# Performance work log

Measured on AMD Instinct MI355X. Metric: run time of the kernel, lower is better.

The kernel has to match this reference:

```python
import jax, jax.numpy as jnp
import numpy as np

DIM = 1024
HIDDEN = 4096
NUM_EXPERTS = 8
TOP_K = 2
T = 8192


def setup_inputs() -> dict:
    key = jax.random.key(0)
    ks = jax.random.split(key, 5)
    scale = 0.02
    x = jax.random.normal(ks[0], (T, DIM), dtype=jnp.float32)
    gate_w = jax.random.normal(ks[1], (NUM_EXPERTS, DIM), dtype=jnp.float32) * scale  # Linear weight [out,in]
    w1 = jax.random.normal(ks[2], (NUM_EXPERTS, HIDDEN, DIM), dtype=jnp.float32) * scale
    w2 = jax.random.normal(ks[3], (NUM_EXPERTS, DIM, HIDDEN), dtype=jnp.float32) * scale
    w3 = jax.random.normal(ks[4], (NUM_EXPERTS, HIDDEN, DIM), dtype=jnp.float32) * scale
    return {"x": x, "gate_w": gate_w, "w1": w1, "w2": w2, "w3": w3}


def reference(x, gate_w, w1, w2, w3):
    # Router: softmax over all experts, take top-2, renormalize.
    logits = jnp.einsum('td,ed->te', x, gate_w)            # [T, E]
    probs = jax.nn.softmax(logits, axis=-1)
    topw, topi = jax.lax.top_k(probs, TOP_K)               # [T, 2]
    topw = topw / jnp.sum(topw, axis=-1, keepdims=True)
    out = jnp.zeros_like(x)
    num_experts = w1.shape[0]
    for e in range(num_experts):
        # combine weight for expert e per token (0 if not routed here)
        w_e = jnp.sum(jnp.where(topi == e, topw, 0.0), axis=-1)   # [T]
        h = jax.nn.silu(x @ w1[e].T) * (x @ w3[e].T)              # [T, HIDDEN]
        out = out + w_e[:, None] * (h @ w2[e].T)                  # [T, DIM]
    return out
```

## Files before the change

### kernel.cpp

```cpp
#include <hip/hip_runtime.h>
#include <hip/hip_bf16.h>
#include <cstdint>
#include <cstddef>

#define TK 8192
#define DIM 1024
#define HID 4096
#define NE 8

#define BK 64
#define NIT1 (DIM / BK)
#define NIT2 (HID / BK)
#define HSZ 4096

typedef __attribute__((ext_vector_type(8))) __bf16 bfrag;
typedef __attribute__((ext_vector_type(4))) float ffrag;

static __device__ __forceinline__ ushort f2bf(float f) {
    union { float f; uint32_t u; } v; v.f = f;
    uint32_t r = (v.u + 0x7fffu + ((v.u >> 16) & 1u)) >> 16;
    return (ushort)r;
}

static __device__ __forceinline__ uint4 pack8(float4 a, float4 b) {
    union { ushort u[8]; uint4 q; } pk;
    pk.u[0] = f2bf(a.x); pk.u[1] = f2bf(a.y); pk.u[2] = f2bf(a.z); pk.u[3] = f2bf(a.w);
    pk.u[4] = f2bf(b.x); pk.u[5] = f2bf(b.y); pk.u[6] = f2bf(b.z); pk.u[7] = f2bf(b.w);
    return pk.q;
}

static __device__ __forceinline__ void gld16(const ushort* g, ushort* l) {
    __builtin_amdgcn_global_load_lds(
        (const __attribute__((address_space(1))) unsigned int*)g,
        (__attribute__((address_space(3))) unsigned int*)l, 16, 0, 0);
}

#define LDSIDX(r, kc) ((((r) >> 3) << 8) + ((kc) << 6) + (((r) & 7) << 3))
#define SLOT_R(s)  ((((s) >> 5) << 3) | ((s) & 7))
#define SLOT_KC(s) (((s) >> 3) & 3)

__global__ __launch_bounds__(256) void k_cvt(const float* __restrict__ src,
                                             ushort* __restrict__ dst, int n8) {
    int i = blockIdx.x * blockDim.x + threadIdx.x;
    if (i >= n8) return;
    const float4* p = (const float4*)src + (size_t)i * 2;
    ((uint4*)dst)[i] = pack8(p[0], p[1]);
}

__global__ __launch_bounds__(256) void k_router(const float* __restrict__ x,
                                                const float* __restrict__ gw,
                                                int* __restrict__ topi, float* __restrict__ topw) {
    int t = blockIdx.x * 4 + (threadIdx.x >> 6);
    int lane = threadIdx.x & 63;
    if (t >= TK) return;
    double acc[NE];
#pragma unroll
    for (int e = 0; e < NE; ++e) acc[e] = 0.0;
    const float* xr = x + (size_t)t * DIM;
    for (int k = lane; k < DIM; k += 64) {
        double xv = (double)xr[k];
#pragma unroll
        for (int e = 0; e < NE; ++e) acc[e] += xv * (double)gw[e * DIM + k];
    }
#pragma unroll
    for (int e = 0; e < NE; ++e) {
#pragma unroll
        for (int off = 32; off > 0; off >>= 1) acc[e] += __shfl_xor(acc[e], off);
    }
    if (lane == 0) {
        int i1 = 0;
#pragma unroll
        for (int e = 1; e < NE; ++e) if (acc[e] > acc[i1]) i1 = e;
        int i2 = (i1 == 0) ? 1 : 0;
#pragma unroll
        for (int e = 0; e < NE; ++e) if (e != i1 && acc[e] > acc[i2]) i2 = e;
        double w = 1.0 / (1.0 + exp(acc[i2] - acc[i1]));
        topi[t * 2 + 0] = i1; topi[t * 2 + 1] = i2;
        topw[t * 2 + 0] = (float)w; topw[t * 2 + 1] = (float)(1.0 - w);
    }
}

__global__ void k_count(const int* __restrict__ topi, int* __restrict__ counts) {
    int i = blockIdx.x * blockDim.x + threadIdx.x;
    if (i < 2 * TK) atomicAdd(&counts[topi[i]], 1);
}

__global__ void k_scan(const int* __restrict__ counts, int* __restrict__ offs,
                       int* __restrict__ cursor, int* __restrict__ desc,
                       int* __restrict__ ndesc) {
    if (threadIdx.x == 0 && blockIdx.x == 0) {
        int s = 0, d = 0;
        for (int e = 0; e < NE; ++e) {
            offs[e] = s; cursor[e] = s;
            int tiles = (counts[e] + 127) >> 7;
            for (int t = 0; t < tiles; ++t) desc[d++] = (e << 16) | t;
            s += counts[e];
        }
        offs[NE] = s;
        ndesc[0] = d;
    }
}

__global__ void k_scatter(const int* __restrict__ topi, const float* __restrict__ topw,
                          int* __restrict__ cursor, int* __restrict__ perm, float* __restrict__ pw) {
    int t = blockIdx.x * blockDim.x + threadIdx.x;
    if (t >= TK) return;
#pragma unroll
    for (int k = 0; k < 2; ++k) {
        int e = topi[t * 2 + k];
        int pos = atomicAdd(&cursor[e], 1);
        perm[pos] = t; pw[pos] = topw[t * 2 + k];
    }
}


__global__ __launch_bounds__(256, 4) void k_ffn1(const ushort* __restrict__ xb,
                                                 const ushort* __restrict__ w1b,
                                                 const ushort* __restrict__ w3b,
                                                 const int* __restrict__ offs,
                                                 const int* __restrict__ perm,
                                                 const int* __restrict__ desc,
                                                 const int* __restrict__ ndesc_g,
                                                 ushort* __restrict__ H) {
    __shared__ ushort lA[2 * HSZ];
    __shared__ ushort lB[2 * HSZ];
    __shared__ int lTok[128];

    const int tid = threadIdx.x;
    const int lane = tid & 63, wid = tid >> 6;
    const int l15 = lane & 15, kcc = lane >> 4;
    const int wm = (wid >> 1) * 64;
    const int wn = (wid & 1) * 64;
    const int gbase = wn >> 4;

    const int nitems = ndesc_g[0] << 6;

    const int r0 = SLOT_R(tid), k0c = SLOT_KC(tid);
    const int r1 = SLOT_R(tid + 256), k1c = SLOT_KC(tid + 256);

    bfrag a[4], b[4];
    ffrag acc[4][4];

#pragma unroll 1
    for (int w = blockIdx.x; w < nitems; w += (int)gridDim.x) {
        __syncthreads();
        const int de = desc[w >> 6];
        const int e = de >> 16, mt = de & 0xffff, nt = w & 63;
        const int m0 = offs[e] + (mt << 7);
        const int nrows = min(128, offs[e + 1] - m0);
        if (tid < 128) lTok[tid] = (tid < nrows) ? perm[m0 + tid] : perm[m0];
        __syncthreads();

        const ushort* pA0 = xb + (size_t)lTok[r0] * DIM + k0c * 8;
        const ushort* pA1 = xb + (size_t)lTok[r1] * DIM + k1c * 8;
        const ushort* pB0;
        const ushort* pB1;
        {
            const size_t ebase = (size_t)e * HID * DIM;
            int gg0 = r0 >> 4, gg1 = r1 >> 4;
            int h0 = nt * 64 + (((gg0 >> 1) << 4) | (r0 & 15));
            int h1 = nt * 64 + (((gg1 >> 1) << 4) | (r1 & 15));
            pB0 = ((gg0 & 1) ? w3b : w1b) + ebase + (size_t)h0 * DIM + k0c * 8;
            pB1 = ((gg1 & 1) ? w3b : w1b) + ebase + (size_t)h1 * DIM + k1c * 8;
        }

#pragma unroll
        for (int i = 0; i < 4; ++i)
#pragma unroll
            for (int j = 0; j < 4; ++j) acc[i][j] = (ffrag)0.f;

#pragma unroll 1
        for (int kt = 0; kt < NIT1; ++kt) {
            const int kb = kt * BK;
#pragma unroll
            for (int h = 0; h < 2; ++h) {
                gld16(pA0 + kb + h * 32, lA + h * HSZ + (wid * 64) * 8);
                gld16(pA1 + kb + h * 32, lA + h * HSZ + (256 + wid * 64) * 8);
                gld16(pB0 + kb + h * 32, lB + h * HSZ + (wid * 64) * 8);
                gld16(pB1 + kb + h * 32, lB + h * HSZ + (256 + wid * 64) * 8);
            }
            __syncthreads();
#pragma unroll
            for (int h = 0; h < 2; ++h) {
                const ushort* A_ = lA + h * HSZ;
                const ushort* B_ = lB + h * HSZ;
#pragma unroll
                for (int j = 0; j < 4; ++j) b[j] = *(const bfrag*)&B_[LDSIDX(wn + j * 16 + l15, kcc)];
#pragma unroll
                for (int i = 0; i < 4; ++i) a[i] = *(const bfrag*)&A_[LDSIDX(wm + i * 16 + l15, kcc)];
                __builtin_amdgcn_s_setprio(1);
#pragma unroll
                for (int i = 0; i < 4; ++i)
#pragma unroll
                    for (int j = 0; j < 4; ++j)
                        acc[i][j] = __builtin_amdgcn_mfma_f32_16x16x32_bf16(a[i], b[j], acc[i][j], 0, 0, 0);
                __builtin_amdgcn_s_setprio(0);
            }
            __syncthreads();
        }

#pragma unroll
        for (int i = 0; i < 4; ++i) {
            int rbase = wm + i * 16 + ((lane >> 4) << 2);
#pragma unroll
            for (int q = 0; q < 4; ++q) {
                int rl = rbase + q;
                if (rl >= nrows) continue;
                size_t rowoff = (size_t)(m0 + rl) * HID;
#pragma unroll
                for (int jf = 0; jf < 4; jf += 2) {
                    int gg = gbase + jf;
                    int col = nt * 64 + ((gg >> 1) << 4) + l15;
                    float h1 = acc[i][jf][q], h3 = acc[i][jf + 1][q];
                    H[rowoff + col] = f2bf((h1 / (1.f + __expf(-h1))) * h3);
                }
            }
        }
    }
}

__global__ __launch_bounds__(256, 4) void k_ffn2(const ushort* __restrict__ H,
                                                 const ushort* __restrict__ w2b,
                                                 const int* __restrict__ offs,
                                                 const int* __restrict__ perm,
                                                 const float* __restrict__ pw,
                                                 const int* __restrict__ desc,
                                                 const int* __restrict__ ndesc_g,
                                                 float* __restrict__ out) {
    __shared__ ushort lA[2 * HSZ];
    __shared__ ushort lB[2 * HSZ];
    __shared__ int lTok[128];
    __shared__ float lPw[128];

    const int tid = threadIdx.x;
    const int lane = tid & 63, wid = tid >> 6;
    const int l15 = lane & 15, kcc = lane >> 4;
    const int wm = (wid >> 1) * 64;
    const int wn = (wid & 1) * 64;

    const int nitems = ndesc_g[0] << 3;

    const int r0 = SLOT_R(tid), k0c = SLOT_KC(tid);
    const int r1 = SLOT_R(tid + 256), k1c = SLOT_KC(tid + 256);

    bfrag a[4], b[4];
    ffrag acc[4][4];

#pragma unroll 1
    for (int w = blockIdx.x; w < nitems; w += (int)gridDim.x) {
        __syncthreads();
        const int de = desc[w >> 3];
        const int e = de >> 16, mt = de & 0xffff, nt = w & 7;
        const int m0 = offs[e] + (mt << 7);
        const int nrows = min(128, offs[e + 1] - m0);
        if (tid < 128) {
            bool v = tid < nrows;
            lTok[tid] = v ? perm[m0 + tid] : 0;
            lPw[tid]  = v ? pw[m0 + tid] : 0.f;
        }
        __syncthreads();

        int p0 = m0 + r0; if (p0 > 2 * TK - 1) p0 = 2 * TK - 1;
        int p1 = m0 + r1; if (p1 > 2 * TK - 1) p1 = 2 * TK - 1;
        const ushort* pA0 = H + (size_t)p0 * HID + k0c * 8;
        const ushort* pA1 = H + (size_t)p1 * HID + k1c * 8;
        const size_t ebase = (size_t)e * DIM * HID;
        const ushort* pB0 = w2b + ebase + (size_t)(nt * 128 + r0) * HID + k0c * 8;
        const ushort* pB1 = w2b + ebase + (size_t)(nt * 128 + r1) * HID + k1c * 8;

#pragma unroll
        for (int i = 0; i < 4; ++i)
#pragma unroll
            for (int j = 0; j < 4; ++j) acc[i][j] = (ffrag)0.f;

#pragma unroll 1
        for (int kt = 0; kt < NIT2; ++kt) {
            const int kb = kt * BK;
#pragma unroll
            for (int h = 0; h < 2; ++h) {
                gld16(pA0 + kb + h * 32, lA + h * HSZ + (wid * 64) * 8);
                gld16(pA1 + kb + h * 32, lA + h * HSZ + (256 + wid * 64) * 8);
                gld16(pB0 + kb + h * 32, lB + h * HSZ + (wid * 64) * 8);
                gld16(pB1 + kb + h * 32, lB + h * HSZ + (256 + wid * 64) * 8);
            }
            __syncthreads();
#pragma unroll
            for (int h = 0; h < 2; ++h) {
                const ushort* A_ = lA + h * HSZ;
                const ushort* B_ = lB + h * HSZ;
#pragma unroll
                for (int j = 0; j < 4; ++j) b[j] = *(const bfrag*)&B_[LDSIDX(wn + j * 16 + l15, kcc)];
#pragma unroll
                for (int i = 0; i < 4; ++i) a[i] = *(const bfrag*)&A_[LDSIDX(wm + i * 16 + l15, kcc)];
                __builtin_amdgcn_s_setprio(1);
#pragma unroll
                for (int i = 0; i < 4; ++i)
#pragma unroll
                    for (int j = 0; j < 4; ++j)
                        acc[i][j] = __builtin_amdgcn_mfma_f32_16x16x32_bf16(a[i], b[j], acc[i][j], 0, 0, 0);
                __builtin_amdgcn_s_setprio(0);
            }
            __syncthreads();
        }

#pragma unroll
        for (int i = 0; i < 4; ++i) {
            int rbase = wm + i * 16 + ((lane >> 4) << 2);
#pragma unroll
            for (int q = 0; q < 4; ++q) {
                int rl = rbase + q;
                if (rl >= nrows) continue;
                int tok = lTok[rl];
                float wgt = lPw[rl];
                size_t rowoff = (size_t)tok * DIM;
#pragma unroll
                for (int j = 0; j < 4; ++j) {
                    int col = nt * 128 + wn + j * 16 + l15;
                    atomicAdd(&out[rowoff + col], acc[i][j][q] * wgt);
                }
            }
        }
    }
}

extern "C" void kernel_launch(void* const* d_in, const int* in_sizes, int n_in,
                              void* d_out, int out_size, void* d_ws, size_t ws_size,
                              hipStream_t stream) {
    const float* x  = (const float*)d_in[0];
    const float* gw = (const float*)d_in[1];
    const float* w1 = (const float*)d_in[2];
    const float* w2 = (const float*)d_in[3];
    const float* w3 = (const float*)d_in[4];
    float* out = (float*)d_out;

    char* ws = (char*)d_ws;
    int*    topi   = (int*)(ws + 0);
    float*  topw   = (float*)(ws + 65536);
    int*    perm   = (int*)(ws + 131072);
    float*  pw     = (float*)(ws + 196608);
    int*    counts = (int*)(ws + 262144);
    int*    offs   = (int*)(ws + 262144 + 256);
    int*    cursor = (int*)(ws + 262144 + 512);
    int*    ndesc  = (int*)(ws + 262144 + 768);
    int*    desc   = (int*)(ws + 262144 + 1024);

    const size_t OFF_XB = 524288;
    const size_t OFF_H  = OFF_XB + 16777216;
    const size_t OFF_WA = OFF_H + 134217728;
    const size_t OFF_WB = OFF_WA + 67108864;

    ushort* xb  = (ushort*)(ws + OFF_XB);
    ushort* H   = (ushort*)(ws + OFF_H);
    ushort* wA  = (ushort*)(ws + OFF_WA);
    ushort* wB  = (ushort*)(ws + OFF_WB);

    hipMemsetAsync(counts, 0, 32, stream);
    hipMemsetAsync(out, 0, (size_t)out_size * sizeof(float), stream);

    k_router<<<dim3(TK / 4), 256, 0, stream>>>(x, gw, topi, topw);
    k_count<<<dim3((2 * TK) / 256), 256, 0, stream>>>(topi, counts);
    k_scan<<<dim3(1), 64, 0, stream>>>(counts, offs, cursor, desc, ndesc);
    k_scatter<<<dim3(TK / 256), 256, 0, stream>>>(topi, topw, cursor, perm, pw);

    k_cvt<<<dim3((TK * DIM / 8) / 256), 256, 0, stream>>>(x, xb, TK * DIM / 8);
    k_cvt<<<dim3((NE * HID * DIM / 8) / 256), 256, 0, stream>>>(w1, wA, NE * HID * DIM / 8);
    k_cvt<<<dim3((NE * HID * DIM / 8) / 256), 256, 0, stream>>>(w3, wB, NE * HID * DIM / 8);

    k_ffn1<<<dim3(1024), 256, 0, stream>>>(xb, wA, wB, offs, perm, desc, ndesc, H);

    k_cvt<<<dim3((NE * DIM * HID / 8) / 256), 256, 0, stream>>>(w2, wA, NE * DIM * HID / 8);

    k_ffn2<<<dim3(1024), 256, 0, stream>>>(H, wA, offs, perm, pw, desc, ndesc, out);
}
```

Measured before the change: 1.185 ms.

## Enlarge MoE GEMM tiles to 512-thread blocks with software-pipelined double-buffered loads

Both expert FFN GEMM kernels move to 512-thread blocks with larger tiles: 256x128 output in the gate/up GEMM and 128x256 in the down GEMM. They now double-buffer LDS and issue global-to-LDS loads for the next K slice while MFMAs run on the current one, using explicit vmcnt waits and raw barriers in place of full __syncthreads. The scan kernel now emits two descriptor lists, one per tile height, and the grid sizes change to match. The aim is to hide memory latency and raise data reuse per block. The cost is more LDS and register pressure, a fragile hand-written wait/barrier schedule, and more padding waste on partial expert tiles.

New measurement: 1.029 ms, median of 2. 1.15x faster.

```diff
diff --git a/kernel.cpp b/kernel.cpp
--- a/kernel.cpp
+++ b/kernel.cpp
@@ -7,11 +7,6 @@
 #define DIM 1024
 #define HID 4096
 #define NE 8
-
-#define BK 64
-#define NIT1 (DIM / BK)
-#define NIT2 (HID / BK)
-#define HSZ 4096
 
 typedef __attribute__((ext_vector_type(8))) __bf16 bfrag;
 typedef __attribute__((ext_vector_type(4))) float ffrag;
@@ -34,6 +29,9 @@
         (const __attribute__((address_space(1))) unsigned int*)g,
         (__attribute__((address_space(3))) unsigned int*)l, 16, 0, 0);
 }
+
+#define BARRIER() asm volatile("s_barrier" ::: "memory")
+#define WAITVM(N) asm volatile("s_waitcnt vmcnt(" #N ")" ::: "memory")
 
 #define LDSIDX(r, kc) ((((r) >> 3) << 8) + ((kc) << 6) + (((r) & 7) << 3))
 #define SLOT_R(s)  ((((s) >> 5) << 3) | ((s) & 7))
@@ -86,18 +84,21 @@
 }
 
 __global__ void k_scan(const int* __restrict__ counts, int* __restrict__ offs,
-                       int* __restrict__ cursor, int* __restrict__ desc,
-                       int* __restrict__ ndesc) {
+                       int* __restrict__ cursor,
+                       int* __restrict__ desc256, int* __restrict__ nd256,
+                       int* __restrict__ desc128, int* __restrict__ nd128) {
     if (threadIdx.x == 0 && blockIdx.x == 0) {
-        int s = 0, d = 0;
+        int s = 0, dA = 0, dB = 0;
         for (int e = 0; e < NE; ++e) {
             offs[e] = s; cursor[e] = s;
-            int tiles = (counts[e] + 127) >> 7;
-            for (int t = 0; t < tiles; ++t) desc[d++] = (e << 16) | t;
+            int tA = (counts[e] + 255) >> 8;
+            for (int t = 0; t < tA; ++t) desc256[dA++] = (e << 16) | t;
+            int tB = (counts[e] + 127) >> 7;
+            for (int t = 0; t < tB; ++t) desc128[dB++] = (e << 16) | t;
             s += counts[e];
         }
         offs[NE] = s;
-        ndesc[0] = d;
+        nd256[0] = dA; nd128[0] = dB;
     }
 }
 
@@ -113,95 +114,118 @@
     }
 }
 
-
-__global__ __launch_bounds__(256, 4) void k_ffn1(const ushort* __restrict__ xb,
+__global__ __launch_bounds__(512, 2) void k_ffn1(const ushort* __restrict__ xb,
                                                  const ushort* __restrict__ w1b,
                                                  const ushort* __restrict__ w3b,
                                                  const int* __restrict__ offs,
                                                  const int* __restrict__ perm,
                                                  const int* __restrict__ desc,
-                                                 const int* __restrict__ ndesc_g,
+                                                 const int* __restrict__ nd_g,
                                                  ushort* __restrict__ H) {
-    __shared__ ushort lA[2 * HSZ];
-    __shared__ ushort lB[2 * HSZ];
-    __shared__ int lTok[128];
+    __shared__ ushort lA[2 * 16384];
+    __shared__ ushort lB[2 * 16384];
+    __shared__ int lTok[256];
 
     const int tid = threadIdx.x;
     const int lane = tid & 63, wid = tid >> 6;
     const int l15 = lane & 15, kcc = lane >> 4;
-    const int wm = (wid >> 1) * 64;
-    const int wn = (wid & 1) * 64;
-    const int gbase = wn >> 4;
-
-    const int nitems = ndesc_g[0] << 6;
-
-    const int r0 = SLOT_R(tid), k0c = SLOT_KC(tid);
-    const int r1 = SLOT_R(tid + 256), k1c = SLOT_KC(tid + 256);
-
-    bfrag a[4], b[4];
-    ffrag acc[4][4];
+    const int mw = wid >> 2;
+    const int wn = (wid & 3) * 64;
+    const int mwoff = mw * 8192;
+    const int wid512 = wid * 512;
+
+    const int NT1 = DIM / 64;
+    const int nitems = nd_g[0] << 5;
+
+    int aoff[4], boff[4];
+#pragma unroll
+    for (int i = 0; i < 4; ++i) aoff[i] = LDSIDX(i * 16 + l15, kcc);
+#pragma unroll
+    for (int j = 0; j < 4; ++j) {
+        int brow = wn + j * 16 + l15;
+        boff[j] = ((brow >> 7) << 13) + LDSIDX(brow & 127, kcc);
+    }
+
+    const int rS = SLOT_R(tid & 511), kcS = SLOT_KC(tid & 511);
+
+    bfrag a[4], br[4][2];
+    ffrag acc[8][4];
 
 #pragma unroll 1
     for (int w = blockIdx.x; w < nitems; w += (int)gridDim.x) {
         __syncthreads();
-        const int de = desc[w >> 6];
-        const int e = de >> 16, mt = de & 0xffff, nt = w & 63;
-        const int m0 = offs[e] + (mt << 7);
-        const int nrows = min(128, offs[e + 1] - m0);
-        if (tid < 128) lTok[tid] = (tid < nrows) ? perm[m0 + tid] : perm[m0];
+        const int de = desc[w >> 5];
+        const int e = de >> 16, mt = de & 0xffff, nt = w & 31;
+        const int m0 = offs[e] + (mt << 8);
+        const int nrows = min(256, offs[e + 1] - m0);
+        if (tid < 256) lTok[tid] = (tid < nrows) ? perm[m0 + tid] : perm[m0];
         __syncthreads();
 
-        const ushort* pA0 = xb + (size_t)lTok[r0] * DIM + k0c * 8;
-        const ushort* pA1 = xb + (size_t)lTok[r1] * DIM + k1c * 8;
-        const ushort* pB0;
-        const ushort* pB1;
+        const ushort* pA_[2]; const ushort* pB_[2];
         {
             const size_t ebase = (size_t)e * HID * DIM;
-            int gg0 = r0 >> 4, gg1 = r1 >> 4;
-            int h0 = nt * 64 + (((gg0 >> 1) << 4) | (r0 & 15));
-            int h1 = nt * 64 + (((gg1 >> 1) << 4) | (r1 & 15));
-            pB0 = ((gg0 & 1) ? w3b : w1b) + ebase + (size_t)h0 * DIM + k0c * 8;
-            pB1 = ((gg1 & 1) ? w3b : w1b) + ebase + (size_t)h1 * DIM + k1c * 8;
-        }
-
-#pragma unroll
-        for (int i = 0; i < 4; ++i)
+#pragma unroll
+            for (int h = 0; h < 2; ++h) {
+                pA_[h] = xb + (size_t)lTok[h * 128 + rS] * DIM + kcS * 8;
+                int brow = h * 128 + rS;
+                int gg = brow >> 4;
+                int hc = nt * 128 + (((gg >> 1) << 4) | (brow & 15));
+                pB_[h] = ((gg & 1) ? w3b : w1b) + ebase + (size_t)hc * DIM + kcS * 8;
+            }
+        }
+
+#pragma unroll
+        for (int i = 0; i < 8; ++i)
 #pragma unroll
             for (int j = 0; j < 4; ++j) acc[i][j] = (ffrag)0.f;
 
+#define SGA1(DB, HH, TT) do { if ((TT) < NT1) { \
+            gld16(pA_[HH] + (TT) * 64,      lA + (DB) * 16384 + (HH) * 8192 + wid512); \
+            gld16(pA_[HH] + (TT) * 64 + 32, lA + (DB) * 16384 + (HH) * 8192 + 4096 + wid512); } } while (0)
+#define SGB1(DB, HH, TT) do { if ((TT) < NT1) { \
+            gld16(pB_[HH] + (TT) * 64,      lB + (DB) * 16384 + (HH) * 8192 + wid512); \
+            gld16(pB_[HH] + (TT) * 64 + 32, lB + (DB) * 16384 + (HH) * 8192 + 4096 + wid512); } } while (0)
+#define RDB1(DB) do { _Pragma("unroll") for (int j = 0; j < 4; ++j) { \
+            br[j][0] = *(const bfrag*)&lB[(DB) * 16384 + boff[j]]; \
+            br[j][1] = *(const bfrag*)&lB[(DB) * 16384 + boff[j] + 4096]; } } while (0)
+#define RDA1(DB, Q, S) do { _Pragma("unroll") for (int i = 0; i < 4; ++i) \
+            a[i] = *(const bfrag*)&lA[(DB) * 16384 + mwoff + (S) * 4096 + (Q) * 2048 + aoff[i]]; } while (0)
+#define MM1(Q, S) do { __builtin_amdgcn_s_setprio(1); \
+            _Pragma("unroll") for (int i = 0; i < 4; ++i) \
+            _Pragma("unroll") for (int j = 0; j < 4; ++j) \
+                acc[(Q) * 4 + i][j] = __builtin_amdgcn_mfma_f32_16x16x32_bf16(a[i], br[j][S], acc[(Q) * 4 + i][j], 0, 0, 0); \
+            __builtin_amdgcn_s_setprio(0); } while (0)
+#define PH1(DB, Q, S, BL, STG, WT) do { \
+            if (BL) RDB1(DB); RDA1(DB, Q, S); STG; WT; BARRIER(); MM1(Q, S); BARRIER(); } while (0)
+
+        SGA1(0, 0, 0); SGA1(0, 1, 0); SGB1(0, 0, 0); SGB1(0, 1, 0);
+        SGB1(1, 0, 1); SGB1(1, 1, 1);
+        WAITVM(4);
+        BARRIER();
+
 #pragma unroll 1
-        for (int kt = 0; kt < NIT1; ++kt) {
-            const int kb = kt * BK;
-#pragma unroll
-            for (int h = 0; h < 2; ++h) {
-                gld16(pA0 + kb + h * 32, lA + h * HSZ + (wid * 64) * 8);
-                gld16(pA1 + kb + h * 32, lA + h * HSZ + (256 + wid * 64) * 8);
-                gld16(pB0 + kb + h * 32, lB + h * HSZ + (wid * 64) * 8);
-                gld16(pB1 + kb + h * 32, lB + h * HSZ + (256 + wid * 64) * 8);
-            }
-            __syncthreads();
-#pragma unroll
-            for (int h = 0; h < 2; ++h) {
-                const ushort* A_ = lA + h * HSZ;
-                const ushort* B_ = lB + h * HSZ;
-#pragma unroll
-                for (int j = 0; j < 4; ++j) b[j] = *(const bfrag*)&B_[LDSIDX(wn + j * 16 + l15, kcc)];
-#pragma unroll
-                for (int i = 0; i < 4; ++i) a[i] = *(const bfrag*)&A_[LDSIDX(wm + i * 16 + l15, kcc)];
-                __builtin_amdgcn_s_setprio(1);
-#pragma unroll
-                for (int i = 0; i < 4; ++i)
-#pragma unroll
-                    for (int j = 0; j < 4; ++j)
-                        acc[i][j] = __builtin_amdgcn_mfma_f32_16x16x32_bf16(a[i], b[j], acc[i][j], 0, 0, 0);
-                __builtin_amdgcn_s_setprio(0);
-            }
-            __syncthreads();
-        }
-
-#pragma unroll
-        for (int i = 0; i < 4; ++i) {
-            int rbase = wm + i * 16 + ((lane >> 4) << 2);
+        for (int it = 0; it < NT1 / 2; ++it) {
+            const int t1 = 2 * it + 1, t2 = 2 * it + 2, t3 = 2 * it + 3;
+            const bool last = (it == NT1 / 2 - 1);
+            PH1(0, 0, 0, 1, SGA1(1, 0, t1), );
+            PH1(0, 1, 0, 0, SGA1(1, 1, t1), );
+            PH1(0, 0, 1, 0, SGB1(0, 0, t2), );
+            PH1(0, 1, 1, 0, SGB1(0, 1, t2), if (last) { WAITVM(0); } else { WAITVM(4); });
+            PH1(1, 0, 0, 1, SGA1(0, 0, t2), );
+            PH1(1, 1, 0, 0, SGA1(0, 1, t2), );
+            PH1(1, 0, 1, 0, SGB1(1, 0, t3), );
+            PH1(1, 1, 1, 0, SGB1(1, 1, t3), if (last) { WAITVM(0); } else { WAITVM(4); });
+        }
+#undef PH1
+#undef MM1
+#undef RDA1
+#undef RDB1
+#undef SGB1
+#undef SGA1
+
+#pragma unroll
+        for (int i = 0; i < 8; ++i) {
+            int rbase = mw * 128 + i * 16 + ((lane >> 4) << 2);
 #pragma unroll
             for (int q = 0; q < 4; ++q) {
                 int rl = rbase + q;
@@ -209,8 +233,8 @@
                 size_t rowoff = (size_t)(m0 + rl) * HID;
 #pragma unroll
                 for (int jf = 0; jf < 4; jf += 2) {
-                    int gg = gbase + jf;
-                    int col = nt * 64 + ((gg >> 1) << 4) + l15;
+                    int gg = (wn >> 4) + jf;
+                    int col = nt * 128 + ((gg >> 1) << 4) + l15;
                     float h1 = acc[i][jf][q], h3 = acc[i][jf + 1][q];
                     H[rowoff + col] = f2bf((h1 / (1.f + __expf(-h1))) * h3);
                 }
@@ -219,38 +243,48 @@
     }
 }
 
-__global__ __launch_bounds__(256, 4) void k_ffn2(const ushort* __restrict__ H,
+__global__ __launch_bounds__(512, 2) void k_ffn2(const ushort* __restrict__ Hs,
                                                  const ushort* __restrict__ w2b,
                                                  const int* __restrict__ offs,
                                                  const int* __restrict__ perm,
                                                  const float* __restrict__ pw,
                                                  const int* __restrict__ desc,
-                                                 const int* __restrict__ ndesc_g,
+                                                 const int* __restrict__ nd_g,
                                                  float* __restrict__ out) {
-    __shared__ ushort lA[2 * HSZ];
-    __shared__ ushort lB[2 * HSZ];
+    __shared__ ushort lA[2 * 8192];
+    __shared__ ushort lB[2 * 16384];
     __shared__ int lTok[128];
     __shared__ float lPw[128];
 
     const int tid = threadIdx.x;
     const int lane = tid & 63, wid = tid >> 6;
     const int l15 = lane & 15, kcc = lane >> 4;
-    const int wm = (wid >> 1) * 64;
-    const int wn = (wid & 1) * 64;
-
-    const int nitems = ndesc_g[0] << 3;
-
-    const int r0 = SLOT_R(tid), k0c = SLOT_KC(tid);
-    const int r1 = SLOT_R(tid + 256), k1c = SLOT_KC(tid + 256);
-
-    bfrag a[4], b[4];
+    const int mw = wid >> 2;
+    const int wn = (wid & 3) * 64;
+    const int wid512 = wid * 512;
+
+    const int NT2 = HID / 64;
+    const int nitems = nd_g[0] << 2;
+
+    int aoff[4], boff[4];
+#pragma unroll
+    for (int i = 0; i < 4; ++i) aoff[i] = LDSIDX(mw * 64 + i * 16 + l15, kcc);
+#pragma unroll
+    for (int j = 0; j < 4; ++j) {
+        int brow = wn + j * 16 + l15;
+        boff[j] = ((brow >> 7) << 13) + LDSIDX(brow & 127, kcc);
+    }
+
+    const int rS = SLOT_R(tid & 511), kcS = SLOT_KC(tid & 511);
+
+    bfrag a[4], br[4][2];
     ffrag acc[4][4];
 
 #pragma unroll 1
     for (int w = blockIdx.x; w < nitems; w += (int)gridDim.x) {
         __syncthreads();
-        const int de = desc[w >> 3];
-        const int e = de >> 16, mt = de & 0xffff, nt = w & 7;
+        const int de = desc[w >> 2];
+        const int e = de >> 16, mt = de & 0xffff, nt = w & 3;
         const int m0 = offs[e] + (mt << 7);
         const int nrows = min(128, offs[e + 1] - m0);
         if (tid < 128) {
@@ -260,52 +294,70 @@
         }
         __syncthreads();
 
-        int p0 = m0 + r0; if (p0 > 2 * TK - 1) p0 = 2 * TK - 1;
-        int p1 = m0 + r1; if (p1 > 2 * TK - 1) p1 = 2 * TK - 1;
-        const ushort* pA0 = H + (size_t)p0 * HID + k0c * 8;
-        const ushort* pA1 = H + (size_t)p1 * HID + k1c * 8;
-        const size_t ebase = (size_t)e * DIM * HID;
-        const ushort* pB0 = w2b + ebase + (size_t)(nt * 128 + r0) * HID + k0c * 8;
-        const ushort* pB1 = w2b + ebase + (size_t)(nt * 128 + r1) * HID + k1c * 8;
+        int posA = m0 + rS; if (posA > 2 * TK - 1) posA = 2 * TK - 1;
+        const ushort* pA_ = Hs + (size_t)posA * HID + kcS * 8;
+        const ushort* pB_[2];
+        {
+            const size_t ebase = (size_t)e * DIM * HID;
+#pragma unroll
+            for (int h = 0; h < 2; ++h)
+                pB_[h] = w2b + ebase + (size_t)(nt * 256 + h * 128 + rS) * HID + kcS * 8;
+        }
 
 #pragma unroll
         for (int i = 0; i < 4; ++i)
 #pragma unroll
             for (int j = 0; j < 4; ++j) acc[i][j] = (ffrag)0.f;
 
+#define SGA2(DB, SUB, TT) do { if ((TT) < NT2) \
+            gld16(pA_ + (TT) * 64 + (SUB) * 32, lA + (DB) * 8192 + (SUB) * 4096 + wid512); } while (0)
+#define SGB2(DB, HH, SUB, TT) do { if ((TT) < NT2) \
+            gld16(pB_[HH] + (TT) * 64 + (SUB) * 32, lB + (DB) * 16384 + (HH) * 8192 + (SUB) * 4096 + wid512); } while (0)
+#define RDB2(DB) do { _Pragma("unroll") for (int j = 0; j < 4; ++j) { \
+            br[j][0] = *(const bfrag*)&lB[(DB) * 16384 + boff[j]]; \
+            br[j][1] = *(const bfrag*)&lB[(DB) * 16384 + boff[j] + 4096]; } } while (0)
+#define RDA2(DB, S) do { _Pragma("unroll") for (int i = 0; i < 4; ++i) \
+            a[i] = *(const bfrag*)&lA[(DB) * 8192 + (S) * 4096 + aoff[i]]; } while (0)
+#define MM2(S) do { __builtin_amdgcn_s_setprio(1); \
+            _Pragma("unroll") for (int i = 0; i < 4; ++i) \
+            _Pragma("unroll") for (int j = 0; j < 4; ++j) \
+                acc[i][j] = __builtin_amdgcn_mfma_f32_16x16x32_bf16(a[i], br[j][S], acc[i][j], 0, 0, 0); \
+            __builtin_amdgcn_s_setprio(0); } while (0)
+
+        SGA2(0, 0, 0); SGA2(0, 1, 0);
+        SGB2(0, 0, 0, 0); SGB2(0, 0, 1, 0); SGB2(0, 1, 0, 0); SGB2(0, 1, 1, 0);
+        SGB2(1, 0, 0, 1); SGB2(1, 0, 1, 1); SGB2(1, 1, 0, 1);
+        WAITVM(3);
+        BARRIER();
+
 #pragma unroll 1
-        for (int kt = 0; kt < NIT2; ++kt) {
-            const int kb = kt * BK;
-#pragma unroll
-            for (int h = 0; h < 2; ++h) {
-                gld16(pA0 + kb + h * 32, lA + h * HSZ + (wid * 64) * 8);
-                gld16(pA1 + kb + h * 32, lA + h * HSZ + (256 + wid * 64) * 8);
-                gld16(pB0 + kb + h * 32, lB + h * HSZ + (wid * 64) * 8);
-                gld16(pB1 + kb + h * 32, lB + h * HSZ + (256 + wid * 64) * 8);
-            }
-            __syncthreads();
-#pragma unroll
-            for (int h = 0; h < 2; ++h) {
-                const ushort* A_ = lA + h * HSZ;
-                const ushort* B_ = lB + h * HSZ;
-#pragma unroll
-                for (int j = 0; j < 4; ++j) b[j] = *(const bfrag*)&B_[LDSIDX(wn + j * 16 + l15, kcc)];
-#pragma unroll
-                for (int i = 0; i < 4; ++i) a[i] = *(const bfrag*)&A_[LDSIDX(wm + i * 16 + l15, kcc)];
-                __builtin_amdgcn_s_setprio(1);
-#pragma unroll
-                for (int i = 0; i < 4; ++i)
-#pragma unroll
-                    for (int j = 0; j < 4; ++j)
-                        acc[i][j] = __builtin_amdgcn_mfma_f32_16x16x32_bf16(a[i], b[j], acc[i][j], 0, 0, 0);
-                __builtin_amdgcn_s_setprio(0);
-            }
-            __syncthreads();
-        }
+        for (int it = 0; it < NT2 / 2; ++it) {
+            const int t1 = 2 * it + 1, t2 = 2 * it + 2, t3 = 2 * it + 3;
+            const bool last = (it == NT2 / 2 - 1);
+            RDB2(0); RDA2(0, 0);
+            SGB2(1, 1, 1, t1); SGA2(1, 0, t1); SGA2(1, 1, t1);
+            BARRIER(); MM2(0); BARRIER();
+            RDA2(0, 1);
+            SGB2(0, 0, 0, t2); SGB2(0, 0, 1, t2); SGB2(0, 1, 0, t2);
+            if (last) { WAITVM(0); } else { WAITVM(3); }
+            BARRIER(); MM2(1); BARRIER();
+            RDB2(1); RDA2(1, 0);
+            SGB2(0, 1, 1, t2); SGA2(0, 0, t2); SGA2(0, 1, t2);
+            BARRIER(); MM2(0); BARRIER();
+            RDA2(1, 1);
+            SGB2(1, 0, 0, t3); SGB2(1, 0, 1, t3); SGB2(1, 1, 0, t3);
+            if (last) { WAITVM(0); } else { WAITVM(3); }
+            BARRIER(); MM2(1); BARRIER();
+        }
+#undef MM2
+#undef RDA2
+#undef RDB2
+#undef SGB2
+#undef SGA2
 
 #pragma unroll
         for (int i = 0; i < 4; ++i) {
-            int rbase = wm + i * 16 + ((lane >> 4) << 2);
+            int rbase = mw * 64 + i * 16 + ((lane >> 4) << 2);
 #pragma unroll
             for (int q = 0; q < 4; ++q) {
                 int rl = rbase + q;
@@ -315,7 +367,7 @@
                 size_t rowoff = (size_t)tok * DIM;
 #pragma unroll
                 for (int j = 0; j < 4; ++j) {
-                    int col = nt * 128 + wn + j * 16 + l15;
+                    int col = nt * 256 + wn + j * 16 + l15;
                     atomicAdd(&out[rowoff + col], acc[i][j][q] * wgt);
                 }
             }
@@ -334,15 +386,17 @@
     float* out = (float*)d_out;
 
     char* ws = (char*)d_ws;
-    int*    topi   = (int*)(ws + 0);
-    float*  topw   = (float*)(ws + 65536);
-    int*    perm   = (int*)(ws + 131072);
-    float*  pw     = (float*)(ws + 196608);
-    int*    counts = (int*)(ws + 262144);
-    int*    offs   = (int*)(ws + 262144 + 256);
-    int*    cursor = (int*)(ws + 262144 + 512);
-    int*    ndesc  = (int*)(ws + 262144 + 768);
-    int*    desc   = (int*)(ws + 262144 + 1024);
+    int*    topi    = (int*)(ws + 0);
+    float*  topw    = (float*)(ws + 65536);
+    int*    perm    = (int*)(ws + 131072);
+    float*  pw      = (float*)(ws + 196608);
+    int*    counts  = (int*)(ws + 262144);
+    int*    offs    = (int*)(ws + 262144 + 256);
+    int*    cursor  = (int*)(ws + 262144 + 512);
+    int*    nd256   = (int*)(ws + 262144 + 768);
+    int*    nd128   = (int*)(ws + 262144 + 772);
+    int*    desc256 = (int*)(ws + 262144 + 1024);
+    int*    desc128 = (int*)(ws + 262144 + 2048);
 
     const size_t OFF_XB = 524288;
     const size_t OFF_H  = OFF_XB + 16777216;
@@ -359,16 +413,16 @@
 
     k_router<<<dim3(TK / 4), 256, 0, stream>>>(x, gw, topi, topw);
     k_count<<<dim3((2 * TK) / 256), 256, 0, stream>>>(topi, counts);
-    k_scan<<<dim3(1), 64, 0, stream>>>(counts, offs, cursor, desc, ndesc);
+    k_scan<<<dim3(1), 64, 0, stream>>>(counts, offs, cursor, desc256, nd256, desc128, nd128);
     k_scatter<<<dim3(TK / 256), 256, 0, stream>>>(topi, topw, cursor, perm, pw);
 
     k_cvt<<<dim3((TK * DIM / 8) / 256), 256, 0, stream>>>(x, xb, TK * DIM / 8);
     k_cvt<<<dim3((NE * HID * DIM / 8) / 256), 256, 0, stream>>>(w1, wA, NE * HID * DIM / 8);
     k_cvt<<<dim3((NE * HID * DIM / 8) / 256), 256, 0, stream>>>(w3, wB, NE * HID * DIM / 8);
 
-    k_ffn1<<<dim3(1024), 256, 0, stream>>>(xb, wA, wB, offs, perm, desc, ndesc, H);
+    k_ffn1<<<dim3(256), 512, 0, stream>>>(xb, wA, wB, offs, perm, desc256, nd256, H);
 
     k_cvt<<<dim3((NE * DIM * HID / 8) / 256), 256, 0, stream>>>(w2, wA, NE * DIM * HID / 8);
 
-    k_ffn2<<<dim3(1024), 256, 0, stream>>>(H, wA, offs, perm, pw, desc, ndesc, out);
-}
+    k_ffn2<<<dim3(512), 512, 0, stream>>>(H, wA, offs, perm, pw, desc128, nd128, out);
+}
```
